# Optimization experiments

Hardware: AMD Instinct MI355X
Metric: run time of the kernel (lower is better)

The kernel has to match this reference:

```python
import jax, jax.numpy as jnp
import numpy as np

TEMPERATURE = 0.1


def setup_inputs() -> dict:
    key = jax.random.key(0)
    kx, kc = jax.random.split(key)
    x = jax.random.normal(kx, (4096, 7), dtype=jnp.float32)
    # Keras 'uniform' initializer default range [-0.05, 0.05]
    cutpoints = jax.random.uniform(kc, (7, 3), dtype=jnp.float32, minval=-0.05, maxval=0.05)
    return {"x": x, "cutpoints": cutpoints}


def reference(x, cutpoints):
    # x: (B, F); cutpoints: (F, D) trainable cut points, D cuts per feature
    B, F = x.shape
    D = cutpoints.shape[1]
    # W = linspace(1, D+1, D+1) -> (D+1,)
    W = jnp.arange(1.0, D + 2.0, dtype=x.dtype)
    cp = jnp.sort(cutpoints, axis=1)                                   # (F, D)
    # b = cumsum([0, -c1, -c2, ...]) per feature -> (F, D+1)
    b = jnp.cumsum(jnp.concatenate([jnp.zeros((F, 1), x.dtype), -cp], axis=1), axis=1)
    # h = X @ W + b, vectorized over all features: (B, F, D+1)
    h = x[:, :, None] * W[None, None, :] + b[None, :, :]
    bins = jax.nn.softmax(h / TEMPERATURE, axis=-1)                     # (B, F, D+1)
    # left-fold Kronecker product across features:
    # kron(a,b)[i, j*K+k] = a[i,j]*b[i,k]  (matches einsum('ij,ik->ijk') + reshape)
    out = bins[:, 0, :]
    for f in range(1, F):
        out = (out[:, :, None] * bins[:, f, :][:, None, :]).reshape(B, -1)
    return out  # (B, (D+1)**F)
```

## Files before the change

kernel.cpp:

```cpp
#include <hip/hip_runtime.h>
#include <hip/hip_bf16.h>

#define TEMP_INV 10.0f

__global__ __launch_bounds__(256) void dtree_kernel(
    const float* __restrict__ x,
    const float* __restrict__ cut,
    float* __restrict__ out)
{
    const int b = blockIdx.x;
    const int t = threadIdx.x;

    __shared__ float sb[7][4];
    __shared__ float prodHi[64];
    __shared__ float prodMid[64];

    if (t < 7) {
        float c0 = cut[t * 3 + 0];
        float c1 = cut[t * 3 + 1];
        float c2 = cut[t * 3 + 2];
        float lo = fminf(c0, c1), hi = fmaxf(c0, c1);
        float m0 = fminf(lo, c2);
        float m2 = fmaxf(hi, c2);
        float m1 = (c0 + c1 + c2) - m0 - m2;

        float xb = x[(size_t)b * 7 + t];
        float h0 = xb;
        float h1 = xb * 2.0f - m0;
        float h2 = xb * 3.0f - (m0 + m1);
        float h3 = xb * 4.0f - (m0 + m1 + m2);
        h0 *= TEMP_INV; h1 *= TEMP_INV; h2 *= TEMP_INV; h3 *= TEMP_INV;
        float mx = fmaxf(fmaxf(h0, h1), fmaxf(h2, h3));
        float e0 = __expf(h0 - mx);
        float e1 = __expf(h1 - mx);
        float e2 = __expf(h2 - mx);
        float e3 = __expf(h3 - mx);
        float inv = 1.0f / (e0 + e1 + e2 + e3);
        sb[t][0] = e0 * inv;
        sb[t][1] = e1 * inv;
        sb[t][2] = e2 * inv;
        sb[t][3] = e3 * inv;
    }
    __syncthreads();

    if (t < 64) {
        prodHi[t] = sb[0][(t >> 4) & 3] * sb[1][(t >> 2) & 3] * sb[2][t & 3];
    } else if (t < 128) {
        int k = t - 64;
        prodMid[k] = sb[3][(k >> 4) & 3] * sb[4][(k >> 2) & 3] * sb[5][k & 3];
    }
    __syncthreads();

    const float4 v6 = make_float4(sb[6][0], sb[6][1], sb[6][2], sb[6][3]);
    float4* __restrict__ o = (float4*)(out + (size_t)b * 16384);

#pragma unroll
    for (int j = 0; j < 16; ++j) {
        int n = j * 256 + t;
        float P = prodHi[n >> 6] * prodMid[n & 63];
        o[n] = make_float4(P * v6.x, P * v6.y, P * v6.z, P * v6.w);
    }
}

extern "C" void kernel_launch(void* const* d_in, const int* in_sizes, int n_in,
                              void* d_out, int out_size, void* d_ws, size_t ws_size,
                              hipStream_t stream) {
    const float* x   = (const float*)d_in[0];
    const float* cut = (const float*)d_in[1];
    float* out = (float*)d_out;
    const int B = in_sizes[0] / 7;
    dtree_kernel<<<B, 256, 0, stream>>>(x, cut, out);
}
```

Before: 255.7 us.

## Process eight rows per block with nontemporal vector stores

Each block now handles eight batch rows instead of one, so the grid shrinks to B/8 blocks and the per-block softmax and partial-product setup is amortized across rows. The output writes use nontemporal vector stores to avoid polluting the cache with the large write-only output, and the prodMid value is hoisted out of the inner loop. The risk is less parallelism per block and longer serial store loops, which could reduce latency hiding on a write-bandwidth-bound kernel.

```diff
diff --git a/kernel.cpp b/kernel.cpp
--- a/kernel.cpp
+++ b/kernel.cpp
@@ -2,29 +2,37 @@
 #include <hip/hip_bf16.h>
 
 #define TEMP_INV 10.0f
+#define RPB 8
+
+typedef float vf4 __attribute__((ext_vector_type(4)));
 
 __global__ __launch_bounds__(256) void dtree_kernel(
     const float* __restrict__ x,
     const float* __restrict__ cut,
-    float* __restrict__ out)
+    float* __restrict__ out,
+    int B)
 {
-    const int b = blockIdx.x;
-    const int t = threadIdx.x;
+    const int t  = threadIdx.x;
+    const int r0 = blockIdx.x * RPB;
 
-    __shared__ float sb[7][4];
-    __shared__ float prodHi[64];
-    __shared__ float prodMid[64];
+    __shared__ float sb[RPB][7][4];
+    __shared__ float prodHi[RPB][64];
+    __shared__ float prodMid[RPB][64];
 
-    if (t < 7) {
-        float c0 = cut[t * 3 + 0];
-        float c1 = cut[t * 3 + 1];
-        float c2 = cut[t * 3 + 2];
+    if (t < RPB * 7) {
+        const int r = t / 7;
+        const int f = t - r * 7;
+        const int row = r0 + r;
+
+        float c0 = cut[f * 3 + 0];
+        float c1 = cut[f * 3 + 1];
+        float c2 = cut[f * 3 + 2];
         float lo = fminf(c0, c1), hi = fmaxf(c0, c1);
         float m0 = fminf(lo, c2);
         float m2 = fmaxf(hi, c2);
         float m1 = (c0 + c1 + c2) - m0 - m2;
 
-        float xb = x[(size_t)b * 7 + t];
+        float xb = (row < B) ? x[(size_t)row * 7 + f] : 0.0f;
         float h0 = xb;
         float h1 = xb * 2.0f - m0;
         float h2 = xb * 3.0f - (m0 + m1);
@@ -36,29 +44,40 @@
         float e2 = __expf(h2 - mx);
         float e3 = __expf(h3 - mx);
         float inv = 1.0f / (e0 + e1 + e2 + e3);
-        sb[t][0] = e0 * inv;
-        sb[t][1] = e1 * inv;
-        sb[t][2] = e2 * inv;
-        sb[t][3] = e3 * inv;
+        sb[r][f][0] = e0 * inv;
+        sb[r][f][1] = e1 * inv;
+        sb[r][f][2] = e2 * inv;
+        sb[r][f][3] = e3 * inv;
     }
     __syncthreads();
 
-    if (t < 64) {
-        prodHi[t] = sb[0][(t >> 4) & 3] * sb[1][(t >> 2) & 3] * sb[2][t & 3];
-    } else if (t < 128) {
-        int k = t - 64;
-        prodMid[k] = sb[3][(k >> 4) & 3] * sb[4][(k >> 2) & 3] * sb[5][k & 3];
+    for (int e = t; e < RPB * 64; e += 256) {
+        int r = e >> 6;
+        int k = e & 63;
+        prodHi[r][k]  = sb[r][0][(k >> 4) & 3] * sb[r][1][(k >> 2) & 3] * sb[r][2][k & 3];
+        prodMid[r][k] = sb[r][3][(k >> 4) & 3] * sb[r][4][(k >> 2) & 3] * sb[r][5][k & 3];
     }
     __syncthreads();
 
-    const float4 v6 = make_float4(sb[6][0], sb[6][1], sb[6][2], sb[6][3]);
-    float4* __restrict__ o = (float4*)(out + (size_t)b * 16384);
-
+    const float pmidSel = 0.0f; (void)pmidSel;
 #pragma unroll
-    for (int j = 0; j < 16; ++j) {
-        int n = j * 256 + t;
-        float P = prodHi[n >> 6] * prodMid[n & 63];
-        o[n] = make_float4(P * v6.x, P * v6.y, P * v6.z, P * v6.w);
+    for (int rr = 0; rr < RPB; ++rr) {
+        const int row = r0 + rr;
+        if (row >= B) break;
+        const float v60 = sb[rr][6][0];
+        const float v61 = sb[rr][6][1];
+        const float v62 = sb[rr][6][2];
+        const float v63 = sb[rr][6][3];
+        const float pmid = prodMid[rr][t & 63];
+        vf4* __restrict__ o = (vf4*)(out + (size_t)row * 16384);
+#pragma unroll
+        for (int j = 0; j < 16; ++j) {
+            const int n = j * 256 + t;
+            const float P = prodHi[rr][n >> 6] * pmid;
+            vf4 v;
+            v.x = P * v60; v.y = P * v61; v.z = P * v62; v.w = P * v63;
+            __builtin_nontemporal_store(v, &o[n]);
+        }
     }
 }
 
@@ -69,5 +88,6 @@
     const float* cut = (const float*)d_in[1];
     float* out = (float*)d_out;
     const int B = in_sizes[0] / 7;
-    dtree_kernel<<<B, 256, 0, stream>>>(x, cut, out);
+    const int grid = (B + RPB - 1) / RPB;
+    dtree_kernel<<<grid, 256, 0, stream>>>(x, cut, out, B);
 }
```

Result: slower. 266.5 us (+4.2%).
